# Kernel tuning notes

Measured on AMD Instinct MI355X. Metric: run time of the kernel, lower is better.

Reference implementation:

```python
import jax, jax.numpy as jnp
import numpy as np

B, T, C, H, E, K, F = 2, 2048, 1024, 16, 8, 2, 2048  # batch, seq, d_model, heads, experts, top_k, d_ffn
EPS = 1e-5


def setup_inputs() -> dict:
    key = jax.random.key(0)
    ks = jax.random.split(key, 6)
    s = 0.02
    return {
        "x": jax.random.normal(ks[0], (B, T, C), jnp.float32),
        "ln1_w": jnp.ones((C,), jnp.float32),
        "c_attn_w": jax.random.normal(ks[1], (C, 3 * C), jnp.float32) * s,
        "c_proj_w": jax.random.normal(ks[2], (C, C), jnp.float32) * s,
        "ln2_w": jnp.ones((C,), jnp.float32),
        "router_w": jax.random.normal(ks[3], (C, E), jnp.float32) * s,
        "w1": jnp.clip(jax.random.normal(ks[4], (C, E * F), jnp.float32) * s, -0.06, 0.06),
        "w2": jnp.clip(jax.random.normal(ks[5], (E * F, C), jnp.float32) * s, -0.06, 0.06),
    }


def layernorm(x, w):
    m = x.mean(-1, keepdims=True)
    v = x.var(-1, keepdims=True)
    return (x - m) * jax.lax.rsqrt(v + EPS) * w


def attention(x, c_attn_w, c_proj_w):
    b, t, c = x.shape
    hd = c // H
    q, k, v = jnp.split(x @ c_attn_w, 3, axis=-1)
    q = q.reshape(b, t, H, hd).transpose(0, 2, 1, 3)  # bhtd
    k = k.reshape(b, t, H, hd).transpose(0, 2, 1, 3)
    v = v.reshape(b, t, H, hd).transpose(0, 2, 1, 3)
    att = jnp.einsum('bhqd,bhkd->bhqk', q, k) / jnp.sqrt(jnp.asarray(hd, x.dtype))
    causal = jnp.tril(jnp.ones((t, t), bool))
    att = jnp.where(causal, att, jnp.asarray(-jnp.inf, att.dtype))
    att = jax.nn.softmax(att, axis=-1)
    y = jnp.einsum('bhqk,bhkd->bhqd', att, v)
    y = y.transpose(0, 2, 1, 3).reshape(b, t, c)
    return y @ c_proj_w


def moe_mlp(x, router_w, w1, w2):
    b, t, c = x.shape
    xf = x.reshape(-1, c)  # (N, C), N = b*t
    router_logits = xf @ router_w  # (N, E)
    probs = jax.nn.softmax(router_logits.astype(jnp.float32), axis=-1)
    rw, sel = jax.lax.top_k(probs, K)  # (N, K)
    rw = rw / rw.sum(axis=-1, keepdims=True)  # norm_topk_prob=True
    rw = rw.astype(x.dtype)
    # expert e uses w1[:, e*F:(e+1)*F] and w2[e*F:(e+1)*F, :]
    w1e = w1.reshape(c, E, F).transpose(1, 0, 2)  # (E, C, F)
    w2e = w2.reshape(E, F, c)  # (E, F, C)
    h = jax.nn.gelu(jnp.einsum('nc,ecf->enf', xf, w1e), approximate=False)
    y_all = jnp.einsum('enf,efc->nec', h, w2e)  # (N, E, C)
    y_sel = jnp.take_along_axis(y_all, sel[:, :, None], axis=1)  # (N, K, C)
    y = (y_sel * rw[:, :, None]).sum(axis=1)
    return y.reshape(b, t, c)


def reference(x, ln1_w, c_attn_w, c_proj_w, ln2_w, router_w, w1, w2):
    x = x + attention(layernorm(x, ln1_w), c_attn_w, c_proj_w)
    x = x + moe_mlp(layernorm(x, ln2_w), router_w, w1, w2)
    return x
```

## Files before the change

### kernel.cpp

```cpp
#include <hip/hip_runtime.h>
#include <hip/hip_bf16.h>

#define BB 2
#define TT 2048
#define CCH 1024
#define HH 16
#define HD 64
#define EE 8
#define FF 2048
#define NTOK (BB*TT)

typedef __bf16 bf16x8 __attribute__((ext_vector_type(8)));
typedef float f32x4 __attribute__((ext_vector_type(4)));
typedef unsigned int u32;
typedef const u32 __attribute__((address_space(1)))* gads;
typedef u32 __attribute__((address_space(3)))* lads;

static __device__ __forceinline__ unsigned short f2bf(float f) {
  union { float f; unsigned u; } v; v.f = f;
  unsigned u = v.u;
  u += 0x7fffu + ((u >> 16) & 1u);
  return (unsigned short)(u >> 16);
}
static __device__ __forceinline__ float bf2f(unsigned short h) {
  union { unsigned u; float f; } v; v.u = ((unsigned)h) << 16;
  return v.f;
}

__global__ __launch_bounds__(256) void k_transpose(const float* __restrict__ in,
    unsigned short* __restrict__ out, int R, int Cc) {
  __shared__ float tile[32][33];
  size_t zoff = (size_t)blockIdx.z * (size_t)R * (size_t)Cc;
  int r0 = blockIdx.y * 32, c0 = blockIdx.x * 32;
  int tx = threadIdx.x, ty = threadIdx.y;
#pragma unroll
  for (int ii = 0; ii < 4; ++ii) {
    int i = ty + ii * 8;
    tile[i][tx] = in[zoff + (size_t)(r0 + i) * Cc + c0 + tx];
  }
  __syncthreads();
#pragma unroll
  for (int ii = 0; ii < 4; ++ii) {
    int i = ty + ii * 8;
    out[zoff + (size_t)(c0 + i) * R + r0 + tx] = f2bf(tile[tx][i]);
  }
}

__global__ __launch_bounds__(256) void k_ln(const float* __restrict__ x,
    const float* __restrict__ w, unsigned short* __restrict__ out) {
  int row = blockIdx.x;
  const float* xr = x + (size_t)row * CCH;
  int tid = threadIdx.x;
  float4 v = *(const float4*)&xr[tid * 4];
  float s = v.x + v.y + v.z + v.w;
  float ss = v.x * v.x + v.y * v.y + v.z * v.z + v.w * v.w;
#pragma unroll
  for (int off = 32; off; off >>= 1) { s += __shfl_xor(s, off); ss += __shfl_xor(ss, off); }
  __shared__ float red[8];
  int wv = tid >> 6, l = tid & 63;
  if (l == 0) { red[wv] = s; red[4 + wv] = ss; }
  __syncthreads();
  s = red[0] + red[1] + red[2] + red[3];
  ss = red[4] + red[5] + red[6] + red[7];
  float mean = s * (1.f / CCH);
  float var = ss * (1.f / CCH) - mean * mean;
  float inv = rsqrtf(var + 1e-5f);
  float4 w4 = *(const float4*)&w[tid * 4];
  ushort4 o;
  o.x = f2bf((v.x - mean) * inv * w4.x);
  o.y = f2bf((v.y - mean) * inv * w4.y);
  o.z = f2bf((v.z - mean) * inv * w4.z);
  o.w = f2bf((v.w - mean) * inv * w4.w);
  *(ushort4*)&out[(size_t)row * CCH + tid * 4] = o;
}

#define CSP 140
#define CFP 70
template<int EPI>
__global__ __launch_bounds__(256, 4) void k_gemm128(
    const unsigned short* __restrict__ A, const unsigned short* __restrict__ BT,
    unsigned short* __restrict__ Cb, float* __restrict__ Cf,
    const float* __restrict__ resid, int M, int N, int K,
    const int* __restrict__ tokarr, const int* __restrict__ slotarr,
    const float* __restrict__ wgtarr, const int* __restrict__ offs,
    const int* __restrict__ counts, const int* __restrict__ tmap)
{
  __shared__ __align__(16) char pool[35840];
  unsigned short* As = (unsigned short*)pool;
  unsigned short* Bs = (unsigned short*)(pool + 16384);

  int mb, nb, e = 0, off = 0, cnt = M;
  if (EPI >= 2) {
    int tm = blockIdx.x;
    if (tm >= tmap[8]) return;
    e = 0;
    while (tm >= tmap[e + 1]) ++e;
    mb = tm - tmap[e];
    nb = blockIdx.y;
    cnt = counts[e]; off = offs[e];
  } else {
    int gx = gridDim.x, gy = gridDim.y;
    int nwg = gx * gy;
    int orig = blockIdx.y * gx + blockIdx.x;
    int q = nwg >> 3, r = nwg & 7;
    int xcd = orig & 7, idx = orig >> 3;
    int wk = (xcd < r ? xcd * (q + 1) : r * (q + 1) + (xcd - r) * q) + idx;
    nb = wk % gy; mb = wk / gy;
  }
  int m0 = mb * 128, n0 = nb * 128;

  int tid = threadIdx.x, l = tid & 63, w = tid >> 6;
  int scol = (((l & 7) ^ ((l >> 3) & 7)) * 8);
  const unsigned short* aptr[4];
  const unsigned short* bptr[4];
  const unsigned short* bbase = BT + (size_t)e * (size_t)N * K;
#pragma unroll
  for (int i = 0; i < 4; ++i) {
    int row = (w * 4 + i) * 8 + (l >> 3);
    int ra;
    if (EPI == 2)      ra = tokarr[off + min(m0 + row, cnt - 1)];
    else if (EPI == 3) ra = off + min(m0 + row, cnt - 1);
    else               ra = m0 + row;
    aptr[i] = A + (size_t)ra * K + scol;
    bptr[i] = bbase + (size_t)(n0 + row) * K + scol;
  }

  int wr = (w >> 1) * 64, wc = (w & 1) * 64;
  int frow = l & 15;
  int fkB = (l >> 4) * 16;
  int swz = (frow & 7) << 4;
  f32x4 acc[4][4] = {};

  for (int k0 = 0; k0 < K; k0 += 64) {
#pragma unroll
    for (int i = 0; i < 4; ++i) {
      int j = w * 4 + i;
      __builtin_amdgcn_global_load_lds((gads)(const void*)(aptr[i] + k0),
                                       (lads)(void*)(As + j * 512), 16, 0, 0);
      __builtin_amdgcn_global_load_lds((gads)(const void*)(bptr[i] + k0),
                                       (lads)(void*)(Bs + j * 512), 16, 0, 0);
    }
    __syncthreads();
    const char* ab = (const char*)As;
    const char* bb = (const char*)Bs;
#pragma unroll
    for (int kk = 0; kk < 2; ++kk) {
      int inr = (kk * 64 + fkB) ^ swz;
      bf16x8 af[4], bfr[4];
#pragma unroll
      for (int mi = 0; mi < 4; ++mi)
        af[mi] = *(const bf16x8*)(ab + (wr + mi * 16 + frow) * 128 + inr);
#pragma unroll
      for (int ni = 0; ni < 4; ++ni)
        bfr[ni] = *(const bf16x8*)(bb + (wc + ni * 16 + frow) * 128 + inr);
#pragma unroll
      for (int mi = 0; mi < 4; ++mi)
#pragma unroll
        for (int ni = 0; ni < 4; ++ni)
          acc[mi][ni] = __builtin_amdgcn_mfma_f32_16x16x32_bf16(af[mi], bfr[ni],
                                                                acc[mi][ni], 0, 0, 0);
    }
    __syncthreads();
  }

  int g4 = (l >> 4) * 4, cl = l & 15;

  if (EPI == 0 || EPI == 2) {
    unsigned short* Cs = (unsigned short*)pool;
#pragma unroll
    for (int mi = 0; mi < 4; ++mi)
#pragma unroll
      for (int ni = 0; ni < 4; ++ni)
#pragma unroll
        for (int r2 = 0; r2 < 4; ++r2) {
          float v = acc[mi][ni][r2];
          if (EPI == 2) v = 0.5f * v * (1.f + erff(v * 0.70710678118654752f));
          Cs[(wr + mi * 16 + g4 + r2) * CSP + wc + ni * 16 + cl] = f2bf(v);
        }
    __syncthreads();
    int row = tid >> 1, c0 = (tid & 1) * 64;
    if (EPI == 0 || m0 + row < cnt) {
      size_t grow = (EPI == 2) ? (size_t)(off + m0 + row) : (size_t)(m0 + row);
      unsigned short* dst = Cb + grow * N + n0 + c0;
#pragma unroll
      for (int j = 0; j < 8; ++j)
        ((uint4*)dst)[j] = *(const uint4*)&Cs[row * CSP + c0 + j * 8];
    }
  } else {
    float* Csf = (float*)pool;
#pragma unroll
    for (int p = 0; p < 2; ++p) {
      __syncthreads();
      if ((w & 1) == p) {
#pragma unroll
        for (int mi = 0; mi < 4; ++mi)
#pragma unroll
          for (int ni = 0; ni < 4; ++ni)
#pragma unroll
            for (int r2 = 0; r2 < 4; ++r2)
              Csf[(wr + mi * 16 + g4 + r2) * CFP + ni * 16 + cl] = acc[mi][ni][r2];
      }
      __syncthreads();
      int row = tid >> 1, c0 = (tid & 1) * 32;
      int gcol = n0 + p * 64 + c0;
      if (EPI == 1) {
        float* dst = Cf + (size_t)(m0 + row) * N + gcol;
        const float* rsd = resid + (size_t)(m0 + row) * N + gcol;
#pragma unroll
        for (int j = 0; j < 8; ++j) {
          float4 v = *(const float4*)&Csf[row * CFP + c0 + j * 4];
          float4 rr = ((const float4*)rsd)[j];
          v.x += rr.x; v.y += rr.y; v.z += rr.z; v.w += rr.w;
          ((float4*)dst)[j] = v;
        }
      } else {
        if (m0 + row < cnt) {
          int fl = off + m0 + row;
          int tok = tokarr[fl], slot = slotarr[fl];
          float wg = wgtarr[fl];
          float* dst = Cf + ((size_t)tok * 2 + slot) * N + gcol;
#pragma unroll
          for (int j = 0; j < 8; ++j) {
            float4 v = *(const float4*)&Csf[row * CFP + c0 + j * 4];
            v.x *= wg; v.y *= wg; v.z *= wg; v.w *= wg;
            ((float4*)dst)[j] = v;
          }
        }
      }
    }
  }
}

__global__ __launch_bounds__(256) void k_attn_mfma(const unsigned short* __restrict__ qkv,
    unsigned short* __restrict__ yout)
{
  int fblk = blockIdx.x;
  int xcd = fblk & 7, s = fblk >> 3;
  int hb = s & 3;
  int h = xcd + 8 * (hb & 1);
  int b = hb >> 1;
  int t = s >> 2, t0 = t & 7, u = t >> 3;
  int qt = (u == 0) ? t0 : (u == 1) ? (15 - t0) : (u == 2) ? (16 + t0) : (31 - t0);
  int q0 = qt * 64;

  int tid = threadIdx.x, l = tid & 63, w = tid >> 6;
  const size_t rs = 3 * CCH;

  __shared__ __align__(16) unsigned short Ks[64][72];
  __shared__ __align__(16) unsigned short VtL[64 * 72];
  __shared__ __align__(16) unsigned short Ps[4][16][72];

  int frow = l & 15, fk = (l >> 4) * 8;
  int g4 = l >> 4;
  int kr = tid >> 2, kc0 = (tid & 3) * 8;
  int vr = tid >> 2, vc0 = (tid & 3) * 16;
  int vphys = (((vr >> 3) + 2 * (tid & 3)) & 7) * 8 + (vr & 7);

  const unsigned short* qp = qkv + (size_t)((size_t)b * TT + q0 + w * 16 + frow) * rs + h * HD;
  bf16x8 qf0 = *(const bf16x8*)&qp[fk];
  bf16x8 qf1 = *(const bf16x8*)&qp[32 + fk];

  f32x4 oacc[4] = {};
  float mrow[4] = {-INFINITY, -INFINITY, -INFINITY, -INFINITY};
  float lrow[4] = {};

  uint4 rk0, rk1, rv0, rv1;
  {
    const unsigned short* kp = qkv + (size_t)((size_t)b * TT + kr) * rs + CCH + h * HD;
    rk0 = *(const uint4*)&kp[kc0];
    rk1 = *(const uint4*)&kp[kc0 + 32];
    const unsigned short* vp = qkv + (size_t)((size_t)b * TT + vr) * rs + 2 * CCH + h * HD + vc0;
    rv0 = *(const uint4*)&vp[0];
    rv1 = *(const uint4*)&vp[8];
  }

  for (int kb = 0; kb <= qt; ++kb) {
    __syncthreads();
    *(uint4*)&Ks[kr][kc0]      = rk0;
    *(uint4*)&Ks[kr][kc0 + 32] = rk1;
    {
      unsigned short tmp[16];
      *(uint4*)&tmp[0] = rv0; *(uint4*)&tmp[8] = rv1;
#pragma unroll
      for (int j = 0; j < 16; ++j) VtL[(vc0 + j) * 72 + vphys] = tmp[j];
    }
    __syncthreads();
    if (kb < qt) {
      int k0n = (kb + 1) * 64;
      const unsigned short* kp = qkv + (size_t)((size_t)b * TT + k0n + kr) * rs + CCH + h * HD;
      rk0 = *(const uint4*)&kp[kc0];
      rk1 = *(const uint4*)&kp[kc0 + 32];
      const unsigned short* vp = qkv + (size_t)((size_t)b * TT + k0n + vr) * rs + 2 * CCH + h * HD + vc0;
      rv0 = *(const uint4*)&vp[0];
      rv1 = *(const uint4*)&vp[8];
    }

    f32x4 sacc[4] = {};
#pragma unroll
    for (int nb = 0; nb < 4; ++nb) {
      bf16x8 kf0 = *(const bf16x8*)&Ks[nb * 16 + frow][fk];
      bf16x8 kf1 = *(const bf16x8*)&Ks[nb * 16 + frow][32 + fk];
      sacc[nb] = __builtin_amdgcn_mfma_f32_16x16x32_bf16(qf0, kf0, sacc[nb], 0, 0, 0);
      sacc[nb] = __builtin_amdgcn_mfma_f32_16x16x32_bf16(qf1, kf1, sacc[nb], 0, 0, 0);
    }

    bool diag = (kb == qt);
    float sv[4][4];
#pragma unroll
    for (int nb = 0; nb < 4; ++nb)
#pragma unroll
      for (int r = 0; r < 4; ++r) {
        float v = sacc[nb][r] * 0.125f;
        if (diag) {
          int ckv = nb * 16 + frow;
          int rq = w * 16 + 4 * g4 + r;
          if (ckv > rq) v = -INFINITY;
        }
        sv[nb][r] = v;
      }
    float fscale[4];
#pragma unroll
    for (int r = 0; r < 4; ++r) {
      float vm = fmaxf(fmaxf(sv[0][r], sv[1][r]), fmaxf(sv[2][r], sv[3][r]));
      vm = fmaxf(vm, __shfl_xor(vm, 1));
      vm = fmaxf(vm, __shfl_xor(vm, 2));
      vm = fmaxf(vm, __shfl_xor(vm, 4));
      vm = fmaxf(vm, __shfl_xor(vm, 8));
      float mnew = fmaxf(mrow[r], vm);
      float f = __expf(mrow[r] - mnew);
      mrow[r] = mnew;
      fscale[r] = f;
      float psum = 0.f;
#pragma unroll
      for (int nb = 0; nb < 4; ++nb) {
        float p = __expf(sv[nb][r] - mnew);
        sv[nb][r] = p;
        psum += p;
      }
      psum += __shfl_xor(psum, 1);
      psum += __shfl_xor(psum, 2);
      psum += __shfl_xor(psum, 4);
      psum += __shfl_xor(psum, 8);
      lrow[r] = lrow[r] * f + psum;
    }
#pragma unroll
    for (int nb = 0; nb < 4; ++nb)
#pragma unroll
      for (int r = 0; r < 4; ++r) {
        oacc[nb][r] *= fscale[r];
        Ps[w][4 * g4 + r][nb * 16 + frow] = f2bf(sv[nb][r]);
      }
#pragma unroll
    for (int ks = 0; ks < 2; ++ks) {
      bf16x8 pa = *(const bf16x8*)&Ps[w][frow][ks * 32 + fk];
#pragma unroll
      for (int nb = 0; nb < 4; ++nb) {
        int vchunk = ((ks * 4 + (l >> 4) + 2 * nb) & 7) * 8;
        bf16x8 vb = *(const bf16x8*)&VtL[(nb * 16 + frow) * 72 + vchunk];
        oacc[nb] = __builtin_amdgcn_mfma_f32_16x16x32_bf16(pa, vb, oacc[nb], 0, 0, 0);
      }
    }
  }

  unsigned short* yo = yout + (size_t)((size_t)b * TT + q0 + w * 16) * CCH + h * HD;
#pragma unroll
  for (int r = 0; r < 4; ++r) {
    float inv = 1.f / lrow[r];
    int row = 4 * g4 + r;
#pragma unroll
    for (int nb = 0; nb < 4; ++nb)
      yo[(size_t)row * CCH + nb * 16 + frow] = f2bf(oacc[nb][r] * inv);
  }
}

__global__ __launch_bounds__(256) void k_router(const float* __restrict__ x2,
    const float* __restrict__ ln2w, const float* __restrict__ rw,
    int* __restrict__ sel, float* __restrict__ selw)
{
  int token = blockIdx.x * 4 + (threadIdx.x >> 6);
  int l = threadIdx.x & 63;
  const float* xr = x2 + (size_t)token * CCH;
  float xv[16];
  float s = 0.f, ss = 0.f;
#pragma unroll
  for (int j = 0; j < 16; ++j) { float v = xr[l * 16 + j]; xv[j] = v; s += v; ss += v * v; }
#pragma unroll
  for (int off = 32; off; off >>= 1) { s += __shfl_xor(s, off); ss += __shfl_xor(ss, off); }
  float mean = s * (1.f / CCH);
  float inv = rsqrtf(ss * (1.f / CCH) - mean * mean + 1e-5f);
  float logit[8] = {};
#pragma unroll
  for (int j = 0; j < 16; ++j) {
    float nv = (xv[j] - mean) * inv * ln2w[l * 16 + j];
    const float* rr = &rw[(size_t)(l * 16 + j) * EE];
#pragma unroll
    for (int e = 0; e < 8; ++e) logit[e] = fmaf(nv, rr[e], logit[e]);
  }
#pragma unroll
  for (int e = 0; e < 8; ++e) {
    float v = logit[e];
#pragma unroll
    for (int off = 32; off; off >>= 1) v += __shfl_xor(v, off);
    logit[e] = v;
  }
  float m1 = logit[0]; int i1 = 0;
#pragma unroll
  for (int e = 1; e < 8; ++e) if (logit[e] > m1) { m1 = logit[e]; i1 = e; }
  float m2 = -INFINITY; int i2 = 0;
#pragma unroll
  for (int e = 0; e < 8; ++e) if (e != i1 && logit[e] > m2) { m2 = logit[e]; i2 = e; }
  if (l == 0) {
    float w1v = 1.f / (1.f + __expf(m2 - m1));
    sel[token * 2] = i1; sel[token * 2 + 1] = i2;
    selw[token * 2] = w1v; selw[token * 2 + 1] = 1.f - w1v;
  }
}

__global__ __launch_bounds__(256) void k_count(const int* __restrict__ sel,
    int* __restrict__ counts_pad)
{
  __shared__ int hist[8];
  int tid = threadIdx.x;
  if (tid < 8) hist[tid] = 0;
  __syncthreads();
  int i = blockIdx.x * 256 + tid;
  atomicAdd(&hist[sel[i]], 1);
  __syncthreads();
  if (tid < 8) atomicAdd(&counts_pad[tid * 16], hist[tid]);
}

__global__ void k_offsets(const int* __restrict__ counts_pad, int* __restrict__ counts,
                          int* __restrict__ offs, int* __restrict__ cursors_pad,
                          int* __restrict__ tmap) {
  if (threadIdx.x == 0 && blockIdx.x == 0) {
    int acc = 0, t = 0;
    tmap[0] = 0;
    for (int e = 0; e < 8; ++e) {
      int c = counts_pad[e * 16];
      counts[e] = c; offs[e] = acc; cursors_pad[e * 16] = acc; acc += c;
      t += (c + 127) >> 7;
      tmap[e + 1] = t;
    }
  }
}

__global__ __launch_bounds__(256) void k_scatter(const int* __restrict__ sel,
    const float* __restrict__ selw, int* __restrict__ cursors_pad,
    int* __restrict__ tokarr, int* __restrict__ slotarr, float* __restrict__ wgtarr)
{
  int t = blockIdx.x * 256 + threadIdx.x;
  int l = threadIdx.x & 63;
#pragma unroll
  for (int s2 = 0; s2 < 2; ++s2) {
    int e = sel[t * 2 + s2];
    int pos = 0;
#pragma unroll
    for (int ex = 0; ex < 8; ++ex) {
      unsigned long long mask = __ballot(e == ex);
      if (e == ex) {
        int leader = __ffsll((long long)mask) - 1;
        int cntw = __popcll(mask);
        int base = 0;
        if (l == leader) base = atomicAdd(&cursors_pad[ex * 16], cntw);
        base = __shfl(base, leader);
        unsigned long long below = (l == 0) ? 0ull : (mask << (64 - l));
        pos = base + __popcll(below);
      }
    }
    tokarr[pos] = t; slotarr[pos] = s2; wgtarr[pos] = selw[t * 2 + s2];
  }
}

__global__ __launch_bounds__(256) void k_combine(const float* __restrict__ x2,
    const float* __restrict__ yp, float* __restrict__ out)
{
  int i = blockIdx.x * 256 + threadIdx.x;
  int n = i >> 8, cw = i & 255;
  float4 a = ((const float4*)x2)[i];
  float4 y0 = ((const float4*)yp)[(size_t)(n * 2) * 256 + cw];
  float4 y1 = ((const float4*)yp)[(size_t)(n * 2 + 1) * 256 + cw];
  float4 o;
  o.x = a.x + y0.x + y1.x;
  o.y = a.y + y0.y + y1.y;
  o.z = a.z + y0.z + y1.z;
  o.w = a.w + y0.w + y1.w;
  ((float4*)out)[i] = o;
}

extern "C" void kernel_launch(void* const* d_in, const int* in_sizes, int n_in,
                              void* d_out, int out_size, void* d_ws, size_t ws_size,
                              hipStream_t stream) {
  const float* x     = (const float*)d_in[0];
  const float* ln1w  = (const float*)d_in[1];
  const float* attnw = (const float*)d_in[2];
  const float* projw = (const float*)d_in[3];
  const float* ln2w  = (const float*)d_in[4];
  const float* routw = (const float*)d_in[5];
  const float* w1    = (const float*)d_in[6];
  const float* w2    = (const float*)d_in[7];
  char* ws = (char*)d_ws;

  unsigned short* attn_wT = (unsigned short*)(ws + 0);
  unsigned short* proj_wT = (unsigned short*)(ws + 6291456);
  unsigned short* w1T     = (unsigned short*)(ws + 8388608);
  unsigned short* w2T     = (unsigned short*)(ws + 41943040);
  unsigned short* xn      = (unsigned short*)(ws + 75497472);
  unsigned short* qkv     = (unsigned short*)(ws + 83886080);
  unsigned short* yattn   = (unsigned short*)(ws + 109051904);
  unsigned short* hbuf    = (unsigned short*)(ws + 83886080);
  float* x2 = (float*)(ws + 117440512);
  float* yp = (float*)(ws + 134217728);
  char* rbase = ws + 167772160;
  int* counts_pad  = (int*)(rbase);
  int* counts      = (int*)(rbase + 512);
  int* cursors_pad = (int*)(rbase + 1024);
  int* offs        = (int*)(rbase + 1536);
  int* tmap        = (int*)(rbase + 1600);
  int* sel         = (int*)(rbase + 2048);
  float* selw      = (float*)(rbase + 2048 + 32768);
  int* tokarr      = (int*)(rbase + 2048 + 65536);
  int* slotarr     = (int*)(rbase + 2048 + 98304);
  float* wgtarr    = (float*)(rbase + 2048 + 131072);
  float* outp = (float*)d_out;

  hipMemsetAsync(counts_pad, 0, 512, stream);

  dim3 tb(32, 8);
  k_transpose<<<dim3(96, 32, 1), tb, 0, stream>>>(attnw, attn_wT, 1024, 3072);
  k_transpose<<<dim3(32, 32, 1), tb, 0, stream>>>(projw, proj_wT, 1024, 1024);
  k_transpose<<<dim3(512, 32, 1), tb, 0, stream>>>(w1, w1T, 1024, 16384);
  k_transpose<<<dim3(32, 64, 8), tb, 0, stream>>>(w2, w2T, 2048, 1024);

  k_ln<<<NTOK, 256, 0, stream>>>(x, ln1w, xn);
  k_gemm128<0><<<dim3(32, 24), 256, 0, stream>>>(xn, attn_wT, qkv, nullptr, nullptr,
      NTOK, 3 * CCH, CCH, nullptr, nullptr, nullptr, nullptr, nullptr, nullptr);
  k_attn_mfma<<<dim3(1024), 256, 0, stream>>>(qkv, yattn);
  k_gemm128<1><<<dim3(32, 8), 256, 0, stream>>>(yattn, proj_wT, nullptr, x2, x,
      NTOK, CCH, CCH, nullptr, nullptr, nullptr, nullptr, nullptr, nullptr);
  k_ln<<<NTOK, 256, 0, stream>>>(x2, ln2w, xn);
  k_router<<<NTOK / 4, 256, 0, stream>>>(x2, ln2w, routw, sel, selw);
  k_count<<<32, 256, 0, stream>>>(sel, counts_pad);
  k_offsets<<<1, 64, 0, stream>>>(counts_pad, counts, offs, cursors_pad, tmap);
  k_scatter<<<NTOK / 256, 256, 0, stream>>>(sel, selw, cursors_pad, tokarr, slotarr, wgtarr);
  k_gemm128<2><<<dim3(72, 16), 256, 0, stream>>>(xn, w1T, hbuf, nullptr, nullptr,
      NTOK, FF, CCH, tokarr, slotarr, wgtarr, offs, counts, tmap);
  k_gemm128<3><<<dim3(72, 8), 256, 0, stream>>>(hbuf, w2T, nullptr, yp, nullptr,
      NTOK, CCH, FF, tokarr, slotarr, wgtarr, offs, counts, tmap);
  k_combine<<<4096, 256, 0, stream>>>(x2, yp, outp);
}
```

Before: 395.1 us.

## Widen GEMM tile to 128x256 and add XCD-aware block remap for MoE GEMMs

The shared GEMM kernel now computes a 128x256 output tile per block: each warp holds two sets of 4x4 accumulators and reuses its A fragments across both N halves. B tiles for both halves are staged in a larger LDS pool, and all grids are halved in the N dimension. The expert GEMMs also gain the XCD-interleaved block remapping already used by the dense GEMMs. The aim is more A-tile reuse per load and better L2 locality. In exchange, accumulator registers double and LDS use grows, which can lower occupancy, and fewer blocks may underfill the GPU.

```diff
diff --git a/kernel.cpp b/kernel.cpp
--- a/kernel.cpp
+++ b/kernel.cpp
@@ -85,18 +85,24 @@
     const float* __restrict__ wgtarr, const int* __restrict__ offs,
     const int* __restrict__ counts, const int* __restrict__ tmap)
 {
-  __shared__ __align__(16) char pool[35840];
+  __shared__ __align__(16) char pool[49152];
   unsigned short* As = (unsigned short*)pool;
   unsigned short* Bs = (unsigned short*)(pool + 16384);
 
   int mb, nb, e = 0, off = 0, cnt = M;
   if (EPI >= 2) {
-    int tm = blockIdx.x;
+    int gx = gridDim.x, gy = gridDim.y;
+    int nwg = gx * gy;
+    int orig = blockIdx.y * gx + blockIdx.x;
+    int q = nwg >> 3, r = nwg & 7;
+    int xcd = orig & 7, idx = orig >> 3;
+    int wk = (xcd < r ? xcd * (q + 1) : r * (q + 1) + (xcd - r) * q) + idx;
+    int tm = wk % gx;
+    nb = wk / gx;
     if (tm >= tmap[8]) return;
     e = 0;
     while (tm >= tmap[e + 1]) ++e;
     mb = tm - tmap[e];
-    nb = blockIdx.y;
     cnt = counts[e]; off = offs[e];
   } else {
     int gx = gridDim.x, gy = gridDim.y;
@@ -107,7 +113,7 @@
     int wk = (xcd < r ? xcd * (q + 1) : r * (q + 1) + (xcd - r) * q) + idx;
     nb = wk % gy; mb = wk / gy;
   }
-  int m0 = mb * 128, n0 = nb * 128;
+  int m0 = mb * 128, n0 = nb * 256;
 
   int tid = threadIdx.x, l = tid & 63, w = tid >> 6;
   int scol = (((l & 7) ^ ((l >> 3) & 7)) * 8);
@@ -124,12 +130,13 @@
     aptr[i] = A + (size_t)ra * K + scol;
     bptr[i] = bbase + (size_t)(n0 + row) * K + scol;
   }
+  const size_t bp1 = (size_t)128 * K;
 
   int wr = (w >> 1) * 64, wc = (w & 1) * 64;
   int frow = l & 15;
   int fkB = (l >> 4) * 16;
   int swz = (frow & 7) << 4;
-  f32x4 acc[4][4] = {};
+  f32x4 acc[2][4][4] = {};
 
   for (int k0 = 0; k0 < K; k0 += 64) {
 #pragma unroll
@@ -139,6 +146,8 @@
                                        (lads)(void*)(As + j * 512), 16, 0, 0);
       __builtin_amdgcn_global_load_lds((gads)(const void*)(bptr[i] + k0),
                                        (lads)(void*)(Bs + j * 512), 16, 0, 0);
+      __builtin_amdgcn_global_load_lds((gads)(const void*)(bptr[i] + bp1 + k0),
+                                       (lads)(void*)(Bs + 8192 + j * 512), 16, 0, 0);
     }
     __syncthreads();
     const char* ab = (const char*)As;
@@ -146,19 +155,23 @@
 #pragma unroll
     for (int kk = 0; kk < 2; ++kk) {
       int inr = (kk * 64 + fkB) ^ swz;
-      bf16x8 af[4], bfr[4];
+      bf16x8 af[4];
 #pragma unroll
       for (int mi = 0; mi < 4; ++mi)
         af[mi] = *(const bf16x8*)(ab + (wr + mi * 16 + frow) * 128 + inr);
 #pragma unroll
-      for (int ni = 0; ni < 4; ++ni)
-        bfr[ni] = *(const bf16x8*)(bb + (wc + ni * 16 + frow) * 128 + inr);
-#pragma unroll
-      for (int mi = 0; mi < 4; ++mi)
+      for (int nh = 0; nh < 2; ++nh) {
+        bf16x8 bfr[4];
 #pragma unroll
         for (int ni = 0; ni < 4; ++ni)
-          acc[mi][ni] = __builtin_amdgcn_mfma_f32_16x16x32_bf16(af[mi], bfr[ni],
-                                                                acc[mi][ni], 0, 0, 0);
+          bfr[ni] = *(const bf16x8*)(bb + nh * 16384 + (wc + ni * 16 + frow) * 128 + inr);
+#pragma unroll
+        for (int mi = 0; mi < 4; ++mi)
+#pragma unroll
+          for (int ni = 0; ni < 4; ++ni)
+            acc[nh][mi][ni] = __builtin_amdgcn_mfma_f32_16x16x32_bf16(af[mi], bfr[ni],
+                                                                      acc[nh][mi][ni], 0, 0, 0);
+      }
     }
     __syncthreads();
   }
@@ -168,62 +181,69 @@
   if (EPI == 0 || EPI == 2) {
     unsigned short* Cs = (unsigned short*)pool;
 #pragma unroll
-    for (int mi = 0; mi < 4; ++mi)
-#pragma unroll
-      for (int ni = 0; ni < 4; ++ni)
-#pragma unroll
-        for (int r2 = 0; r2 < 4; ++r2) {
-          float v = acc[mi][ni][r2];
-          if (EPI == 2) v = 0.5f * v * (1.f + erff(v * 0.70710678118654752f));
-          Cs[(wr + mi * 16 + g4 + r2) * CSP + wc + ni * 16 + cl] = f2bf(v);
-        }
-    __syncthreads();
-    int row = tid >> 1, c0 = (tid & 1) * 64;
-    if (EPI == 0 || m0 + row < cnt) {
-      size_t grow = (EPI == 2) ? (size_t)(off + m0 + row) : (size_t)(m0 + row);
-      unsigned short* dst = Cb + grow * N + n0 + c0;
-#pragma unroll
-      for (int j = 0; j < 8; ++j)
-        ((uint4*)dst)[j] = *(const uint4*)&Cs[row * CSP + c0 + j * 8];
+    for (int nh = 0; nh < 2; ++nh) {
+#pragma unroll
+      for (int mi = 0; mi < 4; ++mi)
+#pragma unroll
+        for (int ni = 0; ni < 4; ++ni)
+#pragma unroll
+          for (int r2 = 0; r2 < 4; ++r2) {
+            float v = acc[nh][mi][ni][r2];
+            if (EPI == 2) v = 0.5f * v * (1.f + erff(v * 0.70710678118654752f));
+            Cs[(wr + mi * 16 + g4 + r2) * CSP + wc + ni * 16 + cl] = f2bf(v);
+          }
+      __syncthreads();
+      int row = tid >> 1, c0 = (tid & 1) * 64;
+      if (EPI == 0 || m0 + row < cnt) {
+        size_t grow = (EPI == 2) ? (size_t)(off + m0 + row) : (size_t)(m0 + row);
+        unsigned short* dst = Cb + grow * N + n0 + nh * 128 + c0;
+#pragma unroll
+        for (int j = 0; j < 8; ++j)
+          ((uint4*)dst)[j] = *(const uint4*)&Cs[row * CSP + c0 + j * 8];
+      }
+      __syncthreads();
     }
   } else {
     float* Csf = (float*)pool;
 #pragma unroll
-    for (int p = 0; p < 2; ++p) {
-      __syncthreads();
-      if ((w & 1) == p) {
-#pragma unroll
-        for (int mi = 0; mi < 4; ++mi)
-#pragma unroll
-          for (int ni = 0; ni < 4; ++ni)
-#pragma unroll
-            for (int r2 = 0; r2 < 4; ++r2)
-              Csf[(wr + mi * 16 + g4 + r2) * CFP + ni * 16 + cl] = acc[mi][ni][r2];
-      }
-      __syncthreads();
-      int row = tid >> 1, c0 = (tid & 1) * 32;
-      int gcol = n0 + p * 64 + c0;
-      if (EPI == 1) {
-        float* dst = Cf + (size_t)(m0 + row) * N + gcol;
-        const float* rsd = resid + (size_t)(m0 + row) * N + gcol;
-#pragma unroll
-        for (int j = 0; j < 8; ++j) {
-          float4 v = *(const float4*)&Csf[row * CFP + c0 + j * 4];
-          float4 rr = ((const float4*)rsd)[j];
-          v.x += rr.x; v.y += rr.y; v.z += rr.z; v.w += rr.w;
-          ((float4*)dst)[j] = v;
+    for (int nh = 0; nh < 2; ++nh) {
+#pragma unroll
+      for (int p = 0; p < 2; ++p) {
+        __syncthreads();
+        if ((w & 1) == p) {
+#pragma unroll
+          for (int mi = 0; mi < 4; ++mi)
+#pragma unroll
+            for (int ni = 0; ni < 4; ++ni)
+#pragma unroll
+              for (int r2 = 0; r2 < 4; ++r2)
+                Csf[(wr + mi * 16 + g4 + r2) * CFP + ni * 16 + cl] = acc[nh][mi][ni][r2];
         }
-      } else {
-        if (m0 + row < cnt) {
-          int fl = off + m0 + row;
-          int tok = tokarr[fl], slot = slotarr[fl];
-          float wg = wgtarr[fl];
-          float* dst = Cf + ((size_t)tok * 2 + slot) * N + gcol;
+        __syncthreads();
+        int row = tid >> 1, c0 = (tid & 1) * 32;
+        int gcol = n0 + nh * 128 + p * 64 + c0;
+        if (EPI == 1) {
+          float* dst = Cf + (size_t)(m0 + row) * N + gcol;
+          const float* rsd = resid + (size_t)(m0 + row) * N + gcol;
 #pragma unroll
           for (int j = 0; j < 8; ++j) {
             float4 v = *(const float4*)&Csf[row * CFP + c0 + j * 4];
-            v.x *= wg; v.y *= wg; v.z *= wg; v.w *= wg;
+            float4 rr = ((const float4*)rsd)[j];
+            v.x += rr.x; v.y += rr.y; v.z += rr.z; v.w += rr.w;
             ((float4*)dst)[j] = v;
+          }
+        } else {
+          if (m0 + row < cnt) {
+            int fl = off + m0 + row;
+            int tok = tokarr[fl], slot = slotarr[fl];
+            float wg = wgtarr[fl];
+            float* dst = Cf + ((size_t)tok * 2 + slot) * N + gcol;
+#pragma unroll
+            for (int j = 0; j < 8; ++j) {
+              float4 v = *(const float4*)&Csf[row * CFP + c0 + j * 4];
+              v.x *= wg; v.y *= wg; v.z *= wg; v.w *= wg;
+              ((float4*)dst)[j] = v;
+            }
           }
         }
       }
@@ -532,19 +552,19 @@
   k_transpose<<<dim3(32, 64, 8), tb, 0, stream>>>(w2, w2T, 2048, 1024);
 
   k_ln<<<NTOK, 256, 0, stream>>>(x, ln1w, xn);
-  k_gemm128<0><<<dim3(32, 24), 256, 0, stream>>>(xn, attn_wT, qkv, nullptr, nullptr,
+  k_gemm128<0><<<dim3(32, 12), 256, 0, stream>>>(xn, attn_wT, qkv, nullptr, nullptr,
       NTOK, 3 * CCH, CCH, nullptr, nullptr, nullptr, nullptr, nullptr, nullptr);
   k_attn_mfma<<<dim3(1024), 256, 0, stream>>>(qkv, yattn);
-  k_gemm128<1><<<dim3(32, 8), 256, 0, stream>>>(yattn, proj_wT, nullptr, x2, x,
+  k_gemm128<1><<<dim3(32, 4), 256, 0, stream>>>(yattn, proj_wT, nullptr, x2, x,
       NTOK, CCH, CCH, nullptr, nullptr, nullptr, nullptr, nullptr, nullptr);
   k_ln<<<NTOK, 256, 0, stream>>>(x2, ln2w, xn);
   k_router<<<NTOK / 4, 256, 0, stream>>>(x2, ln2w, routw, sel, selw);
   k_count<<<32, 256, 0, stream>>>(sel, counts_pad);
   k_offsets<<<1, 64, 0, stream>>>(counts_pad, counts, offs, cursors_pad, tmap);
   k_scatter<<<NTOK / 256, 256, 0, stream>>>(sel, selw, cursors_pad, tokarr, slotarr, wgtarr);
-  k_gemm128<2><<<dim3(72, 16), 256, 0, stream>>>(xn, w1T, hbuf, nullptr, nullptr,
+  k_gemm128<2><<<dim3(72, 8), 256, 0, stream>>>(xn, w1T, hbuf, nullptr, nullptr,
       NTOK, FF, CCH, tokarr, slotarr, wgtarr, offs, counts, tmap);
-  k_gemm128<3><<<dim3(72, 8), 256, 0, stream>>>(hbuf, w2T, nullptr, yp, nullptr,
+  k_gemm128<3><<<dim3(72, 4), 256, 0, stream>>>(hbuf, w2T, nullptr, yp, nullptr,
       NTOK, CCH, FF, tokarr, slotarr, wgtarr, offs, counts, tmap);
   k_combine<<<4096, 256, 0, stream>>>(x2, yp, outp);
 }
```

Result: slower. 561.5 us (median of 2 runs) (+42.1%).
